# Kernel optimization log

Hardware: AMD Instinct MI355X
Metric: run time of the kernel (lower is better)

Reference implementation:

```python
import jax, jax.numpy as jnp
import numpy as np

N_STEPS = 4  # fixed-step dopri5 substeps over [t0, t1]
T0, T1 = 0.0, 1.0
EPS = 1e-5

# Dormand-Prince 5(4) Butcher tableau (5th-order solution weights)
_DP_A = [
    [],
    [1/5],
    [3/40, 9/40],
    [44/45, -56/15, 32/9],
    [19372/6561, -25360/2187, 64448/6561, -212/729],
    [9017/3168, -355/33, 46732/5247, 49/176, -5103/18656],
    [35/384, 0.0, 500/1113, 125/192, -2187/6784, 11/84],
]
_DP_B = [35/384, 0.0, 500/1113, 125/192, -2187/6784, 11/84, 0.0]


def _layernorm(x, g, b):
    mu = jnp.mean(x, axis=-1, keepdims=True)
    var = jnp.var(x, axis=-1, keepdims=True)
    return (x - mu) * jax.lax.rsqrt(var + EPS) * g + b


def build_laplacian(edge_index, edge_attr, num_nodes, ew_w1, ew_b1, ew_w2, ew_b2):
    # learnable edge weights: Linear(1,32) -> ReLU -> Linear(32,1) -> Sigmoid
    h = jax.nn.relu(edge_attr @ ew_w1 + ew_b1)            # [E,32]
    ew = jax.nn.sigmoid(h @ ew_w2 + ew_b2)[:, 0]           # [E]
    row, col = edge_index[0], edge_index[1]
    # add self loops with weight 1
    loop = jnp.arange(num_nodes, dtype=edge_index.dtype)
    row = jnp.concatenate([row, loop])
    col = jnp.concatenate([col, loop])
    ew = jnp.concatenate([ew, jnp.ones((num_nodes,), dtype=ew.dtype)])
    # degree counts edges incident on col (unweighted, as torch_geometric.degree)
    deg = jnp.zeros((num_nodes,), dtype=ew.dtype).at[col].add(1.0)
    dis = jnp.where(deg > 0, deg ** -0.5, 0.0)
    w = dis[row] * ew * dis[col]
    adj = jnp.zeros((num_nodes, num_nodes), dtype=ew.dtype).at[row, col].add(w)
    return jnp.eye(num_nodes, dtype=ew.dtype) - adj


def ode_func(state, L, context, p):
    # state: [B,N,F], L: [N,N], context: [B,F]
    B, N, F = state.shape
    ctx = jnp.broadcast_to(context[:, None, :], (B, N, F))
    x = jnp.concatenate([state, ctx], axis=-1)             # [B,N,2F]
    h = jax.nn.relu(_layernorm(x @ p['td_w1'] + p['td_b1'], p['ln1_g'], p['ln1_b']))
    h = jax.nn.relu(_layernorm(h @ p['td_w2'] + p['td_b2'], p['ln2_g'], p['ln2_b']))
    dhdt_temporal = h @ p['td_w3'] + p['td_b3']            # [B,N,F]
    dcoef = jax.nn.sigmoid(jax.nn.relu(state @ p['df_w1'] + p['df_b1']) @ p['df_w2'] + p['df_b2'])  # [B,N,1]
    Lh = jnp.einsum('ij,bjf->bif', L, state)               # batched diffusion
    return dhdt_temporal - dcoef * Lh


def dopri5_fixed(f, y0, t0, t1, n_steps):
    dt = (t1 - t0) / n_steps

    def step(y, _):
        ks = []
        for i in range(7):
            yi = y
            for j, aij in enumerate(_DP_A[i]):
                if aij != 0.0:
                    yi = yi + dt * aij * ks[j]
            ks.append(f(yi))
        ynew = y
        for bi, ki in zip(_DP_B, ks):
            if bi != 0.0:
                ynew = ynew + dt * bi * ki
        return ynew, None

    y, _ = jax.lax.scan(step, y0, None, length=n_steps)
    return y


def setup_inputs() -> dict:
    key = jax.random.key(0)
    ks = jax.random.split(key, 24)
    B, N, F, H, E = 4, 2048, 256, 512, 65536
    s = lambda k, *shape: jax.random.normal(k, shape, dtype=jnp.float32) * 0.05
    return {
        'state': jax.random.normal(ks[0], (B, N, F), dtype=jnp.float32),
        'context': jax.random.normal(ks[1], (B, F), dtype=jnp.float32),
        'edge_attr': jax.random.uniform(ks[2], (E, 1), dtype=jnp.float32),
        'edge_index': jax.random.randint(ks[3], (2, E), 0, N, dtype=jnp.int32),
        'ew_w1': s(ks[4], 1, 32), 'ew_b1': jnp.zeros((32,), jnp.float32),
        'ew_w2': s(ks[5], 32, 1), 'ew_b2': jnp.zeros((1,), jnp.float32),
        'td_w1': s(ks[6], 2 * F, H), 'td_b1': jnp.zeros((H,), jnp.float32),
        'ln1_g': jnp.ones((H,), jnp.float32), 'ln1_b': jnp.zeros((H,), jnp.float32),
        'td_w2': s(ks[7], H, H), 'td_b2': jnp.zeros((H,), jnp.float32),
        'ln2_g': jnp.ones((H,), jnp.float32), 'ln2_b': jnp.zeros((H,), jnp.float32),
        'td_w3': s(ks[8], H, F), 'td_b3': jnp.zeros((F,), jnp.float32),
        'df_w1': s(ks[9], F, H // 2), 'df_b1': jnp.zeros((H // 2,), jnp.float32),
        'df_w2': s(ks[10], H // 2, 1), 'df_b2': jnp.zeros((1,), jnp.float32),
    }


def reference(state, context, edge_attr, edge_index,
              ew_w1, ew_b1, ew_w2, ew_b2,
              td_w1, td_b1, ln1_g, ln1_b, td_w2, td_b2, ln2_g, ln2_b, td_w3, td_b3,
              df_w1, df_b1, df_w2, df_b2):
    N = state.shape[1]
    L = build_laplacian(edge_index, edge_attr, N, ew_w1, ew_b1, ew_w2, ew_b2)
    p = dict(td_w1=td_w1, td_b1=td_b1, ln1_g=ln1_g, ln1_b=ln1_b,
             td_w2=td_w2, td_b2=td_b2, ln2_g=ln2_g, ln2_b=ln2_b,
             td_w3=td_w3, td_b3=td_b3, df_w1=df_w1, df_b1=df_b1,
             df_w2=df_w2, df_b2=df_b2)
    f = lambda y: ode_func(y, L, context, p)
    return dopri5_fixed(f, state, T0, T1, N_STEPS)
```

## Files before the change

kernel.cpp:

```cpp
#include <hip/hip_runtime.h>
#include <cstddef>
#include <cstdint>

#define N_NODES 2048
#define BATCH   4
#define FDIM    256
#define HDIM    512
#define NEDGE   65536
#define BN_     8192
#define DT      0.25f

typedef __attribute__((ext_vector_type(8))) __bf16 bf16x8;
typedef __attribute__((ext_vector_type(4))) float f32x4;

__device__ __forceinline__ ushort f2bf(float f) {
    union { float f; unsigned u; } v; v.f = f;
    return (ushort)((v.u + 0x7FFF + ((v.u >> 16) & 1)) >> 16);
}
__device__ __forceinline__ float bf2f(ushort u) {
    union { float f; unsigned u; } v; v.u = ((unsigned)u) << 16; return v.f;
}
__device__ __forceinline__ void gload16(const void* g, void* l) {
    __builtin_amdgcn_global_load_lds((const __attribute__((address_space(1))) void*)g,
                                     (__attribute__((address_space(3))) void*)l, 16, 0, 0);
}

__global__ void edge_ew_deg(const float* __restrict__ attr, const int* __restrict__ eidx,
                            const float* __restrict__ w1, const float* __restrict__ b1,
                            const float* __restrict__ w2, const float* __restrict__ b2,
                            float* __restrict__ ew, float* __restrict__ deg) {
    int e = blockIdx.x * blockDim.x + threadIdx.x;
    if (e >= NEDGE) return;
    float a = attr[e];
    float s = b2[0];
#pragma unroll
    for (int k = 0; k < 32; ++k)
        s += fmaxf(fmaf(a, w1[k], b1[k]), 0.f) * w2[k];
    ew[e] = 1.f / (1.f + expf(-s));
    atomicAdd(&deg[eidx[NEDGE + e]], 1.f);
}

__global__ void dis_diag(const float* __restrict__ deg, float* __restrict__ dis,
                         float* __restrict__ L) {
    int n = blockIdx.x * blockDim.x + threadIdx.x;
    if (n >= N_NODES) return;
    float d = deg[n] + 1.f;
    dis[n] = rsqrtf(d);
    L[(size_t)n * N_NODES + n] = 1.f - 1.f / d;
}

__global__ void scatter_L(const int* __restrict__ eidx, const float* __restrict__ ew,
                          const float* __restrict__ dis, float* __restrict__ L) {
    int e = blockIdx.x * blockDim.x + threadIdx.x;
    if (e >= NEDGE) return;
    int r = eidx[e], c = eidx[NEDGE + e];
    atomicAdd(&L[(size_t)r * N_NODES + c], -dis[r] * ew[e] * dis[c]);
}

__global__ void ctxproj_kernel(const float* __restrict__ ctx, const float* __restrict__ w1,
                               const float* __restrict__ b1, float* __restrict__ out) {
    int b = blockIdx.x, h = threadIdx.x;
    const float* W = w1 + (size_t)FDIM * HDIM + h;
    const float* c = ctx + b * FDIM;
    float s = b1[h];
#pragma unroll 4
    for (int k = 0; k < FDIM; ++k)
        s = fmaf(c[k], W[(size_t)k * HDIM], s);
    out[b * HDIM + h] = s;
}

__global__ __launch_bounds__(256)
void transpose_cvt(const float* __restrict__ in, int inStride, ushort* __restrict__ out,
                   int R, int C) {
    __shared__ float tile[64][65];
    int r0 = blockIdx.x * 64, c0 = blockIdx.y * 64;
    int t = threadIdx.x, tr = t >> 4, tc = t & 15;
#pragma unroll
    for (int i = 0; i < 4; ++i) {
        float4 v = *(const float4*)&in[(size_t)(r0 + tr + i * 16) * inStride + c0 + tc * 4];
        tile[tr + i * 16][tc * 4 + 0] = v.x; tile[tr + i * 16][tc * 4 + 1] = v.y;
        tile[tr + i * 16][tc * 4 + 2] = v.z; tile[tr + i * 16][tc * 4 + 3] = v.w;
    }
    __syncthreads();
#pragma unroll
    for (int i = 0; i < 4; ++i) {
        int c = tr + i * 16;
        ushort4 o = make_ushort4(f2bf(tile[tc * 4 + 0][c]), f2bf(tile[tc * 4 + 1][c]),
                                 f2bf(tile[tc * 4 + 2][c]), f2bf(tile[tc * 4 + 3][c]));
        *(ushort4*)&out[(size_t)(c0 + c) * R + r0 + tc * 4] = o;
    }
}

__global__ void cvt_bf16(const float* __restrict__ in, ushort* __restrict__ out) {
    int i = blockIdx.x * blockDim.x + threadIdx.x;
    float4 v = ((const float4*)in)[i];
    ((ushort4*)out)[i] = make_ushort4(f2bf(v.x), f2bf(v.y), f2bf(v.z), f2bf(v.w));
}

__global__ __launch_bounds__(256)
void combine_yi(const float* __restrict__ base,
                const float* p0, const float* p1, const float* p2,
                const float* p3, const float* p4,
                float c0, float c1, float c2, float c3, float c4,
                ushort* __restrict__ yi, ushort* __restrict__ yiT) {
    __shared__ ushort tile[64][68];
    int nb = blockIdx.x * 64, fb = blockIdx.y * 64, b = blockIdx.z;
    int t = threadIdx.x, tr = t >> 4, tc = t & 15;
#pragma unroll
    for (int i = 0; i < 4; ++i) {
        int nl = tr + i * 16;
        size_t fi = (((size_t)(b * N_NODES + nb + nl) * FDIM) + fb + tc * 4) >> 2;
        float4 v = ((const float4*)base)[fi];
        if (p0) { float4 q = ((const float4*)p0)[fi]; v.x = fmaf(c0,q.x,v.x); v.y = fmaf(c0,q.y,v.y); v.z = fmaf(c0,q.z,v.z); v.w = fmaf(c0,q.w,v.w); }
        if (p1) { float4 q = ((const float4*)p1)[fi]; v.x = fmaf(c1,q.x,v.x); v.y = fmaf(c1,q.y,v.y); v.z = fmaf(c1,q.z,v.z); v.w = fmaf(c1,q.w,v.w); }
        if (p2) { float4 q = ((const float4*)p2)[fi]; v.x = fmaf(c2,q.x,v.x); v.y = fmaf(c2,q.y,v.y); v.z = fmaf(c2,q.z,v.z); v.w = fmaf(c2,q.w,v.w); }
        if (p3) { float4 q = ((const float4*)p3)[fi]; v.x = fmaf(c3,q.x,v.x); v.y = fmaf(c3,q.y,v.y); v.z = fmaf(c3,q.z,v.z); v.w = fmaf(c3,q.w,v.w); }
        if (p4) { float4 q = ((const float4*)p4)[fi]; v.x = fmaf(c4,q.x,v.x); v.y = fmaf(c4,q.y,v.y); v.z = fmaf(c4,q.z,v.z); v.w = fmaf(c4,q.w,v.w); }
        ushort4 o = make_ushort4(f2bf(v.x), f2bf(v.y), f2bf(v.z), f2bf(v.w));
        ((ushort4*)yi)[fi] = o;
        tile[nl][tc * 4 + 0] = o.x; tile[nl][tc * 4 + 1] = o.y;
        tile[nl][tc * 4 + 2] = o.z; tile[nl][tc * 4 + 3] = o.w;
    }
    __syncthreads();
#pragma unroll
    for (int i = 0; i < 4; ++i) {
        int fl = tr + i * 16;
        ushort4 o = make_ushort4(tile[tc * 4 + 0][fl], tile[tc * 4 + 1][fl],
                                 tile[tc * 4 + 2][fl], tile[tc * 4 + 3][fl]);
        *(ushort4*)&yiT[((size_t)(b * FDIM + fb + fl) * N_NODES) + nb + tc * 4] = o;
    }
}

template<int BM, int BN, int WM, int WN, int BIAS, int OBF>
__global__ __launch_bounds__(256)
void gemm(const ushort* __restrict__ A, const ushort* __restrict__ BT,
          const float* __restrict__ bias, const float* __restrict__ bias2,
          void* __restrict__ C, int N, int K, long sA, long sB, long sC) {
    constexpr int MR = BM / WM / 16;
    constexpr int NR = BN / WN / 16;
    constexpr int ALD = BM / 32;
    constexpr int BLD = BN / 32;
    __shared__ ushort As[BM * 64];
    __shared__ ushort Bs[BN * 64];
    const ushort* Ag = A + (size_t)blockIdx.z * sA;
    const ushort* Bg = BT + (size_t)blockIdx.z * sB;
    const int tid = threadIdx.x;
    const int lane = tid & 63, wid = tid >> 6;
    const int wn = wid % WN, wm = wid / WN;
    const int r15 = lane & 15, g = lane >> 4;
    const int rowBase = blockIdx.y * BM, colBase = blockIdx.x * BN;

    f32x4 acc[MR][NR];
#pragma unroll
    for (int m = 0; m < MR; ++m)
#pragma unroll
        for (int n = 0; n < NR; ++n) acc[m][n] = (f32x4){0.f, 0.f, 0.f, 0.f};

    for (int k0 = 0; k0 < K; k0 += 64) {
#pragma unroll
        for (int c = 0; c < ALD; ++c) {
            int ci = wid * (ALD * 64) + c * 64 + lane;
            int row = ci >> 3, ch = ci & 7;
            gload16(Ag + (size_t)(rowBase + row) * K + k0 + ((ch ^ (row & 7)) << 3),
                    &As[(wid * (ALD * 64) + c * 64) * 8]);
        }
#pragma unroll
        for (int c = 0; c < BLD; ++c) {
            int ci = wid * (BLD * 64) + c * 64 + lane;
            int row = ci >> 3, ch = ci & 7;
            gload16(Bg + (size_t)(colBase + row) * K + k0 + ((ch ^ (row & 7)) << 3),
                    &Bs[(wid * (BLD * 64) + c * 64) * 8]);
        }
        __syncthreads();
#pragma unroll
        for (int kk = 0; kk < 2; ++kk) {
            bf16x8 af[MR], bfr[NR];
#pragma unroll
            for (int m = 0; m < MR; ++m) {
                int lr = wm * (BM / WM) + m * 16 + r15;
                int off = lr * 128 + ((kk * 64 + g * 16) ^ ((lr & 7) << 4));
                af[m] = *(const bf16x8*)((const char*)As + off);
            }
#pragma unroll
            for (int n = 0; n < NR; ++n) {
                int br = wn * (BN / WN) + n * 16 + r15;
                int off = br * 128 + ((kk * 64 + g * 16) ^ ((br & 7) << 4));
                bfr[n] = *(const bf16x8*)((const char*)Bs + off);
            }
#pragma unroll
            for (int m = 0; m < MR; ++m)
#pragma unroll
                for (int n = 0; n < NR; ++n)
                    acc[m][n] = __builtin_amdgcn_mfma_f32_16x16x32_bf16(
                        af[m], bfr[n], acc[m][n], 0, 0, 0);
        }
        __syncthreads();
    }
#pragma unroll
    for (int m = 0; m < MR; ++m) {
        int row = rowBase + wm * (BM / WM) + m * 16 + g * 4;
#pragma unroll
        for (int n = 0; n < NR; ++n) {
            int col = colBase + wn * (BN / WN) + n * 16 + r15;
            float bv = 0.f;
            if (BIAS == 1) bv = bias[col];
            if (BIAS == 3) bv = (col < HDIM) ? bias[(row >> 11) * HDIM + col]
                                             : bias2[col - HDIM];
#pragma unroll
            for (int r = 0; r < 4; ++r) {
                float v = acc[m][n][r] + bv;
                if (OBF) ((ushort*)C)[(size_t)blockIdx.z * sC + (size_t)(row + r) * N + col] = f2bf(v);
                else     ((float*)C)[(size_t)blockIdx.z * sC + (size_t)(row + r) * N + col] = v;
            }
        }
    }
}

template<int IS>
__global__ __launch_bounds__(256)
void ln_bf(const ushort* __restrict__ in, ushort* __restrict__ out,
           const float* __restrict__ g, const float* __restrict__ b) {
    int row = blockIdx.x, t = threadIdx.x;
    unsigned u = *(const unsigned*)&in[(size_t)row * IS + 2 * t];
    float v0 = bf2f((ushort)(u & 0xffff)), v1 = bf2f((ushort)(u >> 16));
    float s = v0 + v1, s2 = v0 * v0 + v1 * v1;
#pragma unroll
    for (int o = 32; o > 0; o >>= 1) { s += __shfl_down(s, o); s2 += __shfl_down(s2, o); }
    __shared__ float red[8];
    int w = t >> 6;
    if ((t & 63) == 0) { red[w] = s; red[4 + w] = s2; }
    __syncthreads();
    s  = red[0] + red[1] + red[2] + red[3];
    s2 = red[4] + red[5] + red[6] + red[7];
    float mu  = s * (1.f / HDIM);
    float var = fmaf(-mu, mu, s2 * (1.f / HDIM));
    float inv = rsqrtf(var + 1e-5f);
    float n0 = fmaxf(fmaf((v0 - mu) * inv, g[2 * t],     b[2 * t]),     0.f);
    float n1 = fmaxf(fmaf((v1 - mu) * inv, g[2 * t + 1], b[2 * t + 1]), 0.f);
    *(unsigned*)&out[(size_t)row * HDIM + 2 * t] =
        (unsigned)f2bf(n0) | ((unsigned)f2bf(n1) << 16);
}

__global__ __launch_bounds__(256)
void finish2(const ushort* __restrict__ hcat, const float* __restrict__ w2,
             const float* __restrict__ b2, const float* __restrict__ Lh,
             float* __restrict__ ks) {
    int row = blockIdx.x * 4 + (threadIdx.x >> 6);
    int lane = threadIdx.x & 63;
    ushort4 hv = *(const ushort4*)&hcat[(size_t)row * 768 + 512 + lane * 4];
    float4 wv = ((const float4*)w2)[lane];
    float s = fmaxf(bf2f(hv.x), 0.f) * wv.x + fmaxf(bf2f(hv.y), 0.f) * wv.y +
              fmaxf(bf2f(hv.z), 0.f) * wv.z + fmaxf(bf2f(hv.w), 0.f) * wv.w;
#pragma unroll
    for (int o = 32; o > 0; o >>= 1) s += __shfl_xor(s, o);
    float dc = 1.f / (1.f + expf(-(s + b2[0])));
    size_t i = (size_t)row * 64 + lane;
    float4 a = ((const float4*)ks)[i];
    float4 l = ((const float4*)Lh)[i];
    a.x = fmaf(-dc, l.x, a.x); a.y = fmaf(-dc, l.y, a.y);
    a.z = fmaf(-dc, l.z, a.z); a.w = fmaf(-dc, l.w, a.w);
    ((float4*)ks)[i] = a;
}

__global__ void combine_f32(float* __restrict__ out, const float* __restrict__ base,
                            const float* p0, const float* p1, const float* p2,
                            const float* p3, const float* p4,
                            float c0, float c1, float c2, float c3, float c4) {
    int i = blockIdx.x * blockDim.x + threadIdx.x;
    float4 v = ((const float4*)base)[i];
    if (p0) { float4 q = ((const float4*)p0)[i]; v.x = fmaf(c0,q.x,v.x); v.y = fmaf(c0,q.y,v.y); v.z = fmaf(c0,q.z,v.z); v.w = fmaf(c0,q.w,v.w); }
    if (p1) { float4 q = ((const float4*)p1)[i]; v.x = fmaf(c1,q.x,v.x); v.y = fmaf(c1,q.y,v.y); v.z = fmaf(c1,q.z,v.z); v.w = fmaf(c1,q.w,v.w); }
    if (p2) { float4 q = ((const float4*)p2)[i]; v.x = fmaf(c2,q.x,v.x); v.y = fmaf(c2,q.y,v.y); v.z = fmaf(c2,q.z,v.z); v.w = fmaf(c2,q.w,v.w); }
    if (p3) { float4 q = ((const float4*)p3)[i]; v.x = fmaf(c3,q.x,v.x); v.y = fmaf(c3,q.y,v.y); v.z = fmaf(c3,q.z,v.z); v.w = fmaf(c3,q.w,v.w); }
    if (p4) { float4 q = ((const float4*)p4)[i]; v.x = fmaf(c4,q.x,v.x); v.y = fmaf(c4,q.y,v.y); v.z = fmaf(c4,q.z,v.z); v.w = fmaf(c4,q.w,v.w); }
    ((float4*)out)[i] = v;
}

extern "C" void kernel_launch(void* const* d_in, const int* in_sizes, int n_in,
                              void* d_out, int out_size, void* d_ws, size_t ws_size,
                              hipStream_t stream) {
    const float* state      = (const float*)d_in[0];
    const float* context    = (const float*)d_in[1];
    const float* edge_attr  = (const float*)d_in[2];
    const int*   edge_index = (const int*)d_in[3];
    const float* ew_w1 = (const float*)d_in[4];
    const float* ew_b1 = (const float*)d_in[5];
    const float* ew_w2 = (const float*)d_in[6];
    const float* ew_b2 = (const float*)d_in[7];
    const float* td_w1 = (const float*)d_in[8];
    const float* td_b1 = (const float*)d_in[9];
    const float* ln1_g = (const float*)d_in[10];
    const float* ln1_b = (const float*)d_in[11];
    const float* td_w2 = (const float*)d_in[12];
    const float* td_b2 = (const float*)d_in[13];
    const float* ln2_g = (const float*)d_in[14];
    const float* ln2_b = (const float*)d_in[15];
    const float* td_w3 = (const float*)d_in[16];
    const float* td_b3 = (const float*)d_in[17];
    const float* df_w1 = (const float*)d_in[18];
    const float* df_b1 = (const float*)d_in[19];
    const float* df_w2 = (const float*)d_in[20];
    const float* df_b2 = (const float*)d_in[21];
    float* out = (float*)d_out;

    float* ws = (float*)d_ws;
    size_t off = 0;
    auto alloc = [&](size_t nfloats) { float* p = ws + off; off += nfloats; return p; };
    float*  ew    = alloc(NEDGE);
    float*  deg   = alloc(N_NODES);
    float*  dis   = alloc(N_NODES);
    float*  ctxp  = alloc((size_t)BATCH * HDIM);
    float*  L     = alloc((size_t)N_NODES * N_NODES);
    ushort* Lbf   = (ushort*)alloc((size_t)N_NODES * N_NODES / 2);
    float*  y     = alloc((size_t)BN_ * FDIM);
    ushort* yi    = (ushort*)alloc((size_t)BN_ * FDIM / 2);
    ushort* yiT   = (ushort*)alloc((size_t)BN_ * FDIM / 2);
    ushort* hcat  = (ushort*)alloc((size_t)BN_ * 768 / 2);
    ushort* hb1   = (ushort*)alloc((size_t)BN_ * HDIM / 2);
    ushort* h2b   = (ushort*)alloc((size_t)BN_ * HDIM / 2);
    float*  Lh    = alloc((size_t)BN_ * FDIM);
    ushort* wcat  = (ushort*)alloc((size_t)768 * FDIM / 2);
    ushort* w2T   = (ushort*)alloc((size_t)HDIM * HDIM / 2);
    ushort* w3T   = (ushort*)alloc((size_t)FDIM * HDIM / 2);
    float* kb[6];
    for (int s = 0; s < 6; ++s) kb[s] = alloc((size_t)BN_ * FDIM);

    hipMemsetAsync(deg, 0, N_NODES * sizeof(float), stream);
    hipMemsetAsync(L, 0, (size_t)N_NODES * N_NODES * sizeof(float), stream);
    edge_ew_deg<<<NEDGE / 256, 256, 0, stream>>>(edge_attr, edge_index, ew_w1, ew_b1, ew_w2, ew_b2, ew, deg);
    dis_diag<<<N_NODES / 256, 256, 0, stream>>>(deg, dis, L);
    scatter_L<<<NEDGE / 256, 256, 0, stream>>>(edge_index, ew, dis, L);
    cvt_bf16<<<(N_NODES * N_NODES / 4) / 256, 256, 0, stream>>>(L, Lbf);
    ctxproj_kernel<<<BATCH, HDIM, 0, stream>>>(context, td_w1, td_b1, ctxp);
    transpose_cvt<<<dim3(FDIM / 64, HDIM / 64), 256, 0, stream>>>(td_w1, HDIM, wcat, FDIM, HDIM);
    transpose_cvt<<<dim3(FDIM / 64, FDIM / 64), 256, 0, stream>>>(df_w1, FDIM, wcat + (size_t)HDIM * FDIM, FDIM, FDIM);
    transpose_cvt<<<dim3(HDIM / 64, HDIM / 64), 256, 0, stream>>>(td_w2, HDIM, w2T, HDIM, HDIM);
    transpose_cvt<<<dim3(HDIM / 64, FDIM / 64), 256, 0, stream>>>(td_w3, FDIM, w3T, HDIM, FDIM);

    static const double DPA[6][5] = {
        {0, 0, 0, 0, 0},
        {1.0/5, 0, 0, 0, 0},
        {3.0/40, 9.0/40, 0, 0, 0},
        {44.0/45, -56.0/15, 32.0/9, 0, 0},
        {19372.0/6561, -25360.0/2187, 64448.0/6561, -212.0/729, 0},
        {9017.0/3168, -355.0/33, 46732.0/5247, 49.0/176, -5103.0/18656},
    };

    const int NV4 = BN_ * FDIM / 4;
    const float* ycur = state;
    for (int step = 0; step < 4; ++step) {
        for (int s = 0; s < 6; ++s) {
            const float* p[5] = {nullptr, nullptr, nullptr, nullptr, nullptr};
            float c[5] = {0, 0, 0, 0, 0};
            for (int j = 0; j < s; ++j) { p[j] = kb[j]; c[j] = (float)(DT * DPA[s][j]); }
            combine_yi<<<dim3(N_NODES / 64, FDIM / 64, BATCH), 256, 0, stream>>>(
                ycur, p[0], p[1], p[2], p[3], p[4], c[0], c[1], c[2], c[3], c[4], yi, yiT);
            float* ks = kb[s];
            gemm<128, 128, 2, 2, 3, 1><<<dim3(768 / 128, BN_ / 128, 1), 256, 0, stream>>>(
                yi, wcat, ctxp, df_b1, hcat, 768, FDIM, 0, 0, 0);
            ln_bf<768><<<BN_, 256, 0, stream>>>(hcat, hb1, ln1_g, ln1_b);
            gemm<64, 128, 1, 4, 1, 1><<<dim3(HDIM / 128, BN_ / 64, 1), 256, 0, stream>>>(
                hb1, w2T, td_b2, nullptr, h2b, HDIM, HDIM, 0, 0, 0);
            ln_bf<512><<<BN_, 256, 0, stream>>>(h2b, h2b, ln2_g, ln2_b);
            gemm<64, 64, 2, 2, 1, 0><<<dim3(FDIM / 64, BN_ / 64, 1), 256, 0, stream>>>(
                h2b, w3T, td_b3, nullptr, ks, FDIM, HDIM, 0, 0, 0);
            gemm<64, 64, 2, 2, 0, 0><<<dim3(FDIM / 64, N_NODES / 64, BATCH), 256, 0, stream>>>(
                Lbf, yiT, nullptr, nullptr, Lh, FDIM, N_NODES,
                0, (long)N_NODES * FDIM, (long)N_NODES * FDIM);
            finish2<<<BN_ / 4, 256, 0, stream>>>(hcat, df_w2, df_b2, Lh, ks);
        }
        float* dst = (step == 3) ? out : y;
        combine_f32<<<NV4 / 256, 256, 0, stream>>>(dst, ycur,
            kb[0], kb[2], kb[3], kb[4], kb[5],
            (float)(DT * 35.0 / 384), (float)(DT * 500.0 / 1113), (float)(DT * 125.0 / 192),
            (float)(DT * -2187.0 / 6784), (float)(DT * 11.0 / 84));
        ycur = y;
    }
    (void)in_sizes; (void)n_in; (void)out_size; (void)ws_size;
}
```

Before: 2.193 ms.

## Fuse Laplacian GEMM epilogue into k update, store k stages in bf16

Stage derivatives k are now stored in bf16 instead of fp32, which halves the traffic of every combine pass. The Laplacian GEMM treats the batch as a 1024-column N dimension and applies -dcoef*Lh directly into ks in its epilogue. This removes the separate Lh buffer and the finish2 pass, with dcoef computed by a small kernel. The final combine of each step also emits yi/yiT for the next step's first stage, which saves one combine launch per step. The cost is extra bf16 rounding on the k stages and a read-modify-write of ks in the GEMM epilogue.

```diff
diff --git a/kernel.cpp b/kernel.cpp
--- a/kernel.cpp
+++ b/kernel.cpp
@@ -98,11 +98,12 @@
 }
 
 __global__ __launch_bounds__(256)
-void combine_yi(const float* __restrict__ base,
-                const float* p0, const float* p1, const float* p2,
-                const float* p3, const float* p4,
-                float c0, float c1, float c2, float c3, float c4,
-                ushort* __restrict__ yi, ushort* __restrict__ yiT) {
+void combine_all(const float* __restrict__ base,
+                 const ushort* p0, const ushort* p1, const ushort* p2,
+                 const ushort* p3, const ushort* p4,
+                 float c0, float c1, float c2, float c3, float c4,
+                 float* __restrict__ dstf, ushort* __restrict__ yi,
+                 ushort* __restrict__ yiT) {
     __shared__ ushort tile[64][68];
     int nb = blockIdx.x * 64, fb = blockIdx.y * 64, b = blockIdx.z;
     int t = threadIdx.x, tr = t >> 4, tc = t & 15;
@@ -111,17 +112,19 @@
         int nl = tr + i * 16;
         size_t fi = (((size_t)(b * N_NODES + nb + nl) * FDIM) + fb + tc * 4) >> 2;
         float4 v = ((const float4*)base)[fi];
-        if (p0) { float4 q = ((const float4*)p0)[fi]; v.x = fmaf(c0,q.x,v.x); v.y = fmaf(c0,q.y,v.y); v.z = fmaf(c0,q.z,v.z); v.w = fmaf(c0,q.w,v.w); }
-        if (p1) { float4 q = ((const float4*)p1)[fi]; v.x = fmaf(c1,q.x,v.x); v.y = fmaf(c1,q.y,v.y); v.z = fmaf(c1,q.z,v.z); v.w = fmaf(c1,q.w,v.w); }
-        if (p2) { float4 q = ((const float4*)p2)[fi]; v.x = fmaf(c2,q.x,v.x); v.y = fmaf(c2,q.y,v.y); v.z = fmaf(c2,q.z,v.z); v.w = fmaf(c2,q.w,v.w); }
-        if (p3) { float4 q = ((const float4*)p3)[fi]; v.x = fmaf(c3,q.x,v.x); v.y = fmaf(c3,q.y,v.y); v.z = fmaf(c3,q.z,v.z); v.w = fmaf(c3,q.w,v.w); }
-        if (p4) { float4 q = ((const float4*)p4)[fi]; v.x = fmaf(c4,q.x,v.x); v.y = fmaf(c4,q.y,v.y); v.z = fmaf(c4,q.z,v.z); v.w = fmaf(c4,q.w,v.w); }
+        if (p0) { ushort4 q = ((const ushort4*)p0)[fi]; v.x = fmaf(c0,bf2f(q.x),v.x); v.y = fmaf(c0,bf2f(q.y),v.y); v.z = fmaf(c0,bf2f(q.z),v.z); v.w = fmaf(c0,bf2f(q.w),v.w); }
+        if (p1) { ushort4 q = ((const ushort4*)p1)[fi]; v.x = fmaf(c1,bf2f(q.x),v.x); v.y = fmaf(c1,bf2f(q.y),v.y); v.z = fmaf(c1,bf2f(q.z),v.z); v.w = fmaf(c1,bf2f(q.w),v.w); }
+        if (p2) { ushort4 q = ((const ushort4*)p2)[fi]; v.x = fmaf(c2,bf2f(q.x),v.x); v.y = fmaf(c2,bf2f(q.y),v.y); v.z = fmaf(c2,bf2f(q.z),v.z); v.w = fmaf(c2,bf2f(q.w),v.w); }
+        if (p3) { ushort4 q = ((const ushort4*)p3)[fi]; v.x = fmaf(c3,bf2f(q.x),v.x); v.y = fmaf(c3,bf2f(q.y),v.y); v.z = fmaf(c3,bf2f(q.z),v.z); v.w = fmaf(c3,bf2f(q.w),v.w); }
+        if (p4) { ushort4 q = ((const ushort4*)p4)[fi]; v.x = fmaf(c4,bf2f(q.x),v.x); v.y = fmaf(c4,bf2f(q.y),v.y); v.z = fmaf(c4,bf2f(q.z),v.z); v.w = fmaf(c4,bf2f(q.w),v.w); }
+        if (dstf) ((float4*)dstf)[fi] = v;
         ushort4 o = make_ushort4(f2bf(v.x), f2bf(v.y), f2bf(v.z), f2bf(v.w));
-        ((ushort4*)yi)[fi] = o;
+        if (yi) ((ushort4*)yi)[fi] = o;
         tile[nl][tc * 4 + 0] = o.x; tile[nl][tc * 4 + 1] = o.y;
         tile[nl][tc * 4 + 2] = o.z; tile[nl][tc * 4 + 3] = o.w;
     }
     __syncthreads();
+    if (!yiT) return;
 #pragma unroll
     for (int i = 0; i < 4; ++i) {
         int fl = tr + i * 16;
@@ -131,7 +134,7 @@
     }
 }
 
-template<int BM, int BN, int WM, int WN, int BIAS, int OBF>
+template<int BM, int BN, int WM, int WN, int BIAS, int EPI>
 __global__ __launch_bounds__(256)
 void gemm(const ushort* __restrict__ A, const ushort* __restrict__ BT,
           const float* __restrict__ bias, const float* __restrict__ bias2,
@@ -196,6 +199,27 @@
         }
         __syncthreads();
     }
+    if (EPI == 2) {
+        int b = colBase >> 8;
+        ushort* ks = (ushort*)C;
+#pragma unroll
+        for (int m = 0; m < MR; ++m) {
+            int row = rowBase + wm * (BM / WM) + m * 16 + g * 4;
+            float4 dcv = *(const float4*)&bias2[b * N_NODES + row];
+            float dca[4] = {dcv.x, dcv.y, dcv.z, dcv.w};
+#pragma unroll
+            for (int n = 0; n < NR; ++n) {
+                int col = colBase + wn * (BN / WN) + n * 16 + r15;
+                int f = col & 255;
+#pragma unroll
+                for (int r = 0; r < 4; ++r) {
+                    size_t idx = ((size_t)(b * N_NODES + row + r)) * 256 + f;
+                    ks[idx] = f2bf(bf2f(ks[idx]) - dca[r] * acc[m][n][r]);
+                }
+            }
+        }
+        return;
+    }
 #pragma unroll
     for (int m = 0; m < MR; ++m) {
         int row = rowBase + wm * (BM / WM) + m * 16 + g * 4;
@@ -209,8 +233,8 @@
 #pragma unroll
             for (int r = 0; r < 4; ++r) {
                 float v = acc[m][n][r] + bv;
-                if (OBF) ((ushort*)C)[(size_t)blockIdx.z * sC + (size_t)(row + r) * N + col] = f2bf(v);
-                else     ((float*)C)[(size_t)blockIdx.z * sC + (size_t)(row + r) * N + col] = v;
+                if (EPI == 1) ((ushort*)C)[(size_t)blockIdx.z * sC + (size_t)(row + r) * N + col] = f2bf(v);
+                else          ((float*)C)[(size_t)blockIdx.z * sC + (size_t)(row + r) * N + col] = v;
             }
         }
     }
@@ -242,9 +266,8 @@
 }
 
 __global__ __launch_bounds__(256)
-void finish2(const ushort* __restrict__ hcat, const float* __restrict__ w2,
-             const float* __restrict__ b2, const float* __restrict__ Lh,
-             float* __restrict__ ks) {
+void dcoef_kernel(const ushort* __restrict__ hcat, const float* __restrict__ w2,
+                  const float* __restrict__ b2, float* __restrict__ dc) {
     int row = blockIdx.x * 4 + (threadIdx.x >> 6);
     int lane = threadIdx.x & 63;
     ushort4 hv = *(const ushort4*)&hcat[(size_t)row * 768 + 512 + lane * 4];
@@ -253,27 +276,7 @@
               fmaxf(bf2f(hv.z), 0.f) * wv.z + fmaxf(bf2f(hv.w), 0.f) * wv.w;
 #pragma unroll
     for (int o = 32; o > 0; o >>= 1) s += __shfl_xor(s, o);
-    float dc = 1.f / (1.f + expf(-(s + b2[0])));
-    size_t i = (size_t)row * 64 + lane;
-    float4 a = ((const float4*)ks)[i];
-    float4 l = ((const float4*)Lh)[i];
-    a.x = fmaf(-dc, l.x, a.x); a.y = fmaf(-dc, l.y, a.y);
-    a.z = fmaf(-dc, l.z, a.z); a.w = fmaf(-dc, l.w, a.w);
-    ((float4*)ks)[i] = a;
-}
-
-__global__ void combine_f32(float* __restrict__ out, const float* __restrict__ base,
-                            const float* p0, const float* p1, const float* p2,
-                            const float* p3, const float* p4,
-                            float c0, float c1, float c2, float c3, float c4) {
-    int i = blockIdx.x * blockDim.x + threadIdx.x;
-    float4 v = ((const float4*)base)[i];
-    if (p0) { float4 q = ((const float4*)p0)[i]; v.x = fmaf(c0,q.x,v.x); v.y = fmaf(c0,q.y,v.y); v.z = fmaf(c0,q.z,v.z); v.w = fmaf(c0,q.w,v.w); }
-    if (p1) { float4 q = ((const float4*)p1)[i]; v.x = fmaf(c1,q.x,v.x); v.y = fmaf(c1,q.y,v.y); v.z = fmaf(c1,q.z,v.z); v.w = fmaf(c1,q.w,v.w); }
-    if (p2) { float4 q = ((const float4*)p2)[i]; v.x = fmaf(c2,q.x,v.x); v.y = fmaf(c2,q.y,v.y); v.z = fmaf(c2,q.z,v.z); v.w = fmaf(c2,q.w,v.w); }
-    if (p3) { float4 q = ((const float4*)p3)[i]; v.x = fmaf(c3,q.x,v.x); v.y = fmaf(c3,q.y,v.y); v.z = fmaf(c3,q.z,v.z); v.w = fmaf(c3,q.w,v.w); }
-    if (p4) { float4 q = ((const float4*)p4)[i]; v.x = fmaf(c4,q.x,v.x); v.y = fmaf(c4,q.y,v.y); v.z = fmaf(c4,q.z,v.z); v.w = fmaf(c4,q.w,v.w); }
-    ((float4*)out)[i] = v;
+    if (lane == 0) dc[row] = 1.f / (1.f + expf(-(s + b2[0])));
 }
 
 extern "C" void kernel_launch(void* const* d_in, const int* in_sizes, int n_in,
@@ -310,6 +313,7 @@
     float*  deg   = alloc(N_NODES);
     float*  dis   = alloc(N_NODES);
     float*  ctxp  = alloc((size_t)BATCH * HDIM);
+    float*  dc    = alloc(BN_);
     float*  L     = alloc((size_t)N_NODES * N_NODES);
     ushort* Lbf   = (ushort*)alloc((size_t)N_NODES * N_NODES / 2);
     float*  y     = alloc((size_t)BN_ * FDIM);
@@ -318,12 +322,11 @@
     ushort* hcat  = (ushort*)alloc((size_t)BN_ * 768 / 2);
     ushort* hb1   = (ushort*)alloc((size_t)BN_ * HDIM / 2);
     ushort* h2b   = (ushort*)alloc((size_t)BN_ * HDIM / 2);
-    float*  Lh    = alloc((size_t)BN_ * FDIM);
     ushort* wcat  = (ushort*)alloc((size_t)768 * FDIM / 2);
     ushort* w2T   = (ushort*)alloc((size_t)HDIM * HDIM / 2);
     ushort* w3T   = (ushort*)alloc((size_t)FDIM * HDIM / 2);
-    float* kb[6];
-    for (int s = 0; s < 6; ++s) kb[s] = alloc((size_t)BN_ * FDIM);
+    ushort* kb[6];
+    for (int s = 0; s < 6; ++s) kb[s] = (ushort*)alloc((size_t)BN_ * FDIM / 2);
 
     hipMemsetAsync(deg, 0, N_NODES * sizeof(float), stream);
     hipMemsetAsync(L, 0, (size_t)N_NODES * N_NODES * sizeof(float), stream);
@@ -346,34 +349,40 @@
         {9017.0/3168, -355.0/33, 46732.0/5247, 49.0/176, -5103.0/18656},
     };
 
-    const int NV4 = BN_ * FDIM / 4;
+    const dim3 cgrid(N_NODES / 64, FDIM / 64, BATCH);
     const float* ycur = state;
     for (int step = 0; step < 4; ++step) {
         for (int s = 0; s < 6; ++s) {
-            const float* p[5] = {nullptr, nullptr, nullptr, nullptr, nullptr};
-            float c[5] = {0, 0, 0, 0, 0};
-            for (int j = 0; j < s; ++j) { p[j] = kb[j]; c[j] = (float)(DT * DPA[s][j]); }
-            combine_yi<<<dim3(N_NODES / 64, FDIM / 64, BATCH), 256, 0, stream>>>(
-                ycur, p[0], p[1], p[2], p[3], p[4], c[0], c[1], c[2], c[3], c[4], yi, yiT);
-            float* ks = kb[s];
+            if (s == 0) {
+                if (step == 0)
+                    combine_all<<<cgrid, 256, 0, stream>>>(ycur, nullptr, nullptr, nullptr,
+                        nullptr, nullptr, 0, 0, 0, 0, 0, nullptr, yi, yiT);
+            } else {
+                const ushort* p[5] = {nullptr, nullptr, nullptr, nullptr, nullptr};
+                float c[5] = {0, 0, 0, 0, 0};
+                for (int j = 0; j < s; ++j) { p[j] = kb[j]; c[j] = (float)(DT * DPA[s][j]); }
+                combine_all<<<cgrid, 256, 0, stream>>>(ycur, p[0], p[1], p[2], p[3], p[4],
+                    c[0], c[1], c[2], c[3], c[4], nullptr, yi, yiT);
+            }
+            ushort* ks = kb[s];
             gemm<128, 128, 2, 2, 3, 1><<<dim3(768 / 128, BN_ / 128, 1), 256, 0, stream>>>(
                 yi, wcat, ctxp, df_b1, hcat, 768, FDIM, 0, 0, 0);
             ln_bf<768><<<BN_, 256, 0, stream>>>(hcat, hb1, ln1_g, ln1_b);
+            dcoef_kernel<<<BN_ / 4, 256, 0, stream>>>(hcat, df_w2, df_b2, dc);
             gemm<64, 128, 1, 4, 1, 1><<<dim3(HDIM / 128, BN_ / 64, 1), 256, 0, stream>>>(
                 hb1, w2T, td_b2, nullptr, h2b, HDIM, HDIM, 0, 0, 0);
             ln_bf<512><<<BN_, 256, 0, stream>>>(h2b, h2b, ln2_g, ln2_b);
-            gemm<64, 64, 2, 2, 1, 0><<<dim3(FDIM / 64, BN_ / 64, 1), 256, 0, stream>>>(
+            gemm<64, 64, 2, 2, 1, 1><<<dim3(FDIM / 64, BN_ / 64, 1), 256, 0, stream>>>(
                 h2b, w3T, td_b3, nullptr, ks, FDIM, HDIM, 0, 0, 0);
-            gemm<64, 64, 2, 2, 0, 0><<<dim3(FDIM / 64, N_NODES / 64, BATCH), 256, 0, stream>>>(
-                Lbf, yiT, nullptr, nullptr, Lh, FDIM, N_NODES,
-                0, (long)N_NODES * FDIM, (long)N_NODES * FDIM);
-            finish2<<<BN_ / 4, 256, 0, stream>>>(hcat, df_w2, df_b2, Lh, ks);
-        }
-        float* dst = (step == 3) ? out : y;
-        combine_f32<<<NV4 / 256, 256, 0, stream>>>(dst, ycur,
+            gemm<64, 64, 2, 2, 0, 2><<<dim3(1024 / 64, N_NODES / 64, 1), 256, 0, stream>>>(
+                Lbf, yiT, nullptr, dc, ks, 1024, N_NODES, 0, 0, 0);
+        }
+        float* dstf = (step == 3) ? out : y;
+        combine_all<<<cgrid, 256, 0, stream>>>(ycur,
             kb[0], kb[2], kb[3], kb[4], kb[5],
             (float)(DT * 35.0 / 384), (float)(DT * 500.0 / 1113), (float)(DT * 125.0 / 192),
-            (float)(DT * -2187.0 / 6784), (float)(DT * 11.0 / 84));
+            (float)(DT * -2187.0 / 6784), (float)(DT * 11.0 / 84),
+            dstf, (step == 3) ? nullptr : yi, (step == 3) ? nullptr : yiT);
         ycur = y;
     }
     (void)in_sizes; (void)n_in; (void)out_size; (void)ws_size;
```

After: 2.115 ms. 1.04x faster.
